# Kernel tuning notes

Hardware: AMD Instinct MI355X
Metric: run time of the kernel (lower is better)

## Reference

```python
import jax, jax.numpy as jnp
import numpy as np

# Module constants (match init_kwargs)
G = 8        # number of channel groups (len(list_input_dim))
D = 16       # per-group input dim
L = 1024     # sequence length
B = 16       # batch
E = 8        # num_experts
OUT = 64     # out_channels
KS = 3       # emb_kernel_size
K = 4        # hardcoded self.k in Channel_Embedding
LOSS_COEF = 0.01


def setup_inputs() -> dict:
    key = jax.random.key(0)
    k0, k1, k2, k3 = jax.random.split(key, 4)
    x = jax.random.normal(k0, (B, G * D, L), jnp.float32)
    # torch inits w_gate to zeros (degenerate); use small random weights for meaningful routing
    w_gate = jax.random.normal(k1, (G, D * 5, E), jnp.float32) * 0.1
    conv1_w = jax.random.normal(k2, (G, OUT, D, KS), jnp.float32) * (1.0 / np.sqrt(D * KS))
    conv1_b = jnp.zeros((G, OUT), jnp.float32)
    conv2_w = jax.random.normal(k3, (G, OUT * E, OUT, 1), jnp.float32) * (1.0 / np.sqrt(OUT))
    conv2_b = jnp.zeros((G, OUT * E), jnp.float32)
    return dict(x=x, w_gate=w_gate, conv1_w=conv1_w, conv1_b=conv1_b,
                conv2_w=conv2_w, conv2_b=conv2_b)


def _cv_squared(v):
    # torch: x.float().var() (unbiased) / (mean^2 + eps)
    v = v.astype(jnp.float32)
    return jnp.var(v, ddof=1) / (jnp.mean(v) ** 2 + 1e-10)


def _conv1d(x, w, b):
    # x [B,C,L], w [O,I,K] -> [B,O,L'] (VALID, stride 1)
    y = jax.lax.conv_general_dilated(x, w, (1,), 'VALID',
                                     dimension_numbers=('NCH', 'OIH', 'NCH'))
    return y + b[None, :, None]


def _group_forward(xg, wg, c1w, c1b, c2w, c2b):
    # xg: [B, D, L] single channel group
    Bb = xg.shape[0]
    # gating input: last timesteps [-6:-1] -> [B, D*5]
    gate_in = xg[:, :, -6:-1].reshape(Bb, -1)
    logits = jax.nn.softmax(gate_in @ wg, axis=1)           # [B, E]
    top_v, top_i = jax.lax.top_k(logits, min(K + 1, E))     # [B, K+1]
    tkv, tki = top_v[:, :K], top_i[:, :K]
    gk = tkv / (tkv.sum(1, keepdims=True) + 1e-6)
    gates = jnp.zeros_like(logits).at[jnp.arange(Bb)[:, None], tki].set(gk)  # [B, E]
    load = (gates > 0).sum(0)                               # eval path: _gates_to_load
    loss = _cv_squared(gates.sum(0)) + _cv_squared(load)
    # experts: conv(D->OUT, k=KS) -> tanh -> conv(OUT -> OUT*E, k=1)
    h = jnp.tanh(_conv1d(xg, c1w, c1b))
    raw = _conv1d(h, c2w, c2b)                              # [B, OUT*E, L']
    Lp = raw.shape[-1]
    # channel index = d*E + e (matches torch permute+reshape(B,-1,OUT,E))
    moe = jnp.einsum('bdel,be->bdl', raw.reshape(Bb, OUT, E, Lp), gates)  # [B, OUT, L']
    return moe, loss, gates


def reference(x, w_gate, conv1_w, conv1_b, conv2_w, conv2_b):
    # split channels into G groups of D: [G, B, D, L]
    xg = x.reshape(x.shape[0], G, D, x.shape[-1]).transpose(1, 0, 2, 3)
    moe, loss, gates = jax.vmap(_group_forward)(xg, w_gate, conv1_w, conv1_b, conv2_w, conv2_b)
    combine_features = moe.transpose(1, 0, 2, 3)   # [B, G, OUT, L']
    out_loss = LOSS_COEF * loss.sum()
    gates_out = gates.transpose(1, 2, 0)           # [B, E, G]
    return combine_features, out_loss, gates_out
```

## Files before the change

### kernel.cpp

```cpp
#include <hip/hip_runtime.h>
#include <hip/hip_bf16.h>

#define NG   8
#define ND   16
#define NL   1024
#define NB   16
#define NE   8
#define NOUT 64
#define NKS  3
#define NK   4
#define NLP  1022

#define OUT_LOSS  (NB*NG*NOUT*NLP)
#define OUT_GATES (OUT_LOSS + 1)

typedef short bf16x8 __attribute__((ext_vector_type(8)));
typedef float f32x4  __attribute__((ext_vector_type(4)));

__device__ __forceinline__ float tanh_fast(float x) {
    float e = exp2f(x * 2.885390081777927f);
    return 1.0f - 2.0f / (e + 1.0f);
}

__device__ __forceinline__ unsigned fbits(float a) { return __builtin_bit_cast(unsigned, a); }
__device__ __forceinline__ float resid(float a) {
    return a - __builtin_bit_cast(float, fbits(a) & 0xFFFF0000u);
}
__device__ __forceinline__ int pack2(float a, float b) {
    return (int)((fbits(a) >> 16) | (fbits(b) & 0xFFFF0000u));
}

__device__ __forceinline__ void compute_gates_f(
    const float* __restrict__ x, const float* __restrict__ wg,
    int g, int b, float gates[8])
{
    float gi[80];
    const float* xrow = x + (size_t)(b * 128 + g * 16) * 1024 + (1024 - 6);
    #pragma unroll
    for (int d = 0; d < 16; ++d) {
        #pragma unroll
        for (int tt = 0; tt < 5; ++tt) gi[d * 5 + tt] = xrow[d * 1024 + tt];
    }
    float lg[8];
    #pragma unroll
    for (int e = 0; e < 8; ++e) lg[e] = 0.f;
    const float* wgg = wg + g * 640;
    #pragma unroll
    for (int j = 0; j < 80; ++j) {
        const float v = gi[j];
        #pragma unroll
        for (int e = 0; e < 8; ++e) lg[e] = fmaf(v, wgg[j * 8 + e], lg[e]);
    }
    float mx = lg[0];
    #pragma unroll
    for (int e = 1; e < 8; ++e) mx = fmaxf(mx, lg[e]);
    float s = 0.f;
    #pragma unroll
    for (int e = 0; e < 8; ++e) { lg[e] = expf(lg[e] - mx); s += lg[e]; }
    const float invsm = 1.f / s;
    #pragma unroll
    for (int e = 0; e < 8; ++e) lg[e] *= invsm;

    int used = 0;
    float tv[4]; int ti[4];
    #pragma unroll
    for (int k = 0; k < 4; ++k) {
        float bv = -1.f; int be = 0;
        #pragma unroll
        for (int e = 0; e < 8; ++e) {
            if (!((used >> e) & 1) && lg[e] > bv) { bv = lg[e]; be = e; }
        }
        tv[k] = bv; ti[k] = be; used |= (1 << be);
    }
    const float s4 = tv[0] + tv[1] + tv[2] + tv[3];
    const float invs = 1.f / (s4 + 1e-6f);
    #pragma unroll
    for (int e = 0; e < 8; ++e) {
        float v = 0.f;
        #pragma unroll
        for (int k = 0; k < 4; ++k) if (ti[k] == e) v = tv[k] * invs;
        gates[e] = v;
    }
}

__global__ __launch_bounds__(256) void prep_kernel(
    const float* __restrict__ x,   const float* __restrict__ wg,
    const float* __restrict__ c1w, const float* __restrict__ c2w,
    const float* __restrict__ c2b,
    float* __restrict__ out, int4* __restrict__ weffA,
    float* __restrict__ beff, float* __restrict__ w1r)
{
    const int bid = blockIdx.x;
    const int t   = threadIdx.x;

    __shared__ float glds[128][8];
    __shared__ float impa[64], loda[64];
    __shared__ float lossg[8];

    if (bid < 128) {
        const int gb = bid, g = gb >> 4, b = gb & 15;
        float gt[8];
        compute_gates_f(x, wg, g, b, gt);

        const int o  = t >> 2;
        const int iq = (t & 3) * 16;
        const float* w2g = c2w + (size_t)g * 512 * 64 + (size_t)o * 8 * 64 + iq;
        float acc[16];
        #pragma unroll
        for (int q = 0; q < 16; ++q) acc[q] = 0.f;
        #pragma unroll
        for (int e = 0; e < 8; ++e) {
            const float4* src = (const float4*)(w2g + e * 64);
            #pragma unroll
            for (int q = 0; q < 4; ++q) {
                float4 v = src[q];
                acc[q*4+0] = fmaf(gt[e], v.x, acc[q*4+0]);
                acc[q*4+1] = fmaf(gt[e], v.y, acc[q*4+1]);
                acc[q*4+2] = fmaf(gt[e], v.z, acc[q*4+2]);
                acc[q*4+3] = fmaf(gt[e], v.w, acc[q*4+3]);
            }
        }
        const int mt  = o >> 4;
        const int ks  = iq >> 5;
        const int lgA = (iq & 31) >> 3;
        int4* wdst = weffA + gb * 1024 + mt * 128 + ks * 64;
        #pragma unroll
        for (int R = 0; R < 2; ++R) {
            int4 whi, wlo;
            whi.x = pack2(acc[R*8+0], acc[R*8+1]);
            whi.y = pack2(acc[R*8+2], acc[R*8+3]);
            whi.z = pack2(acc[R*8+4], acc[R*8+5]);
            whi.w = pack2(acc[R*8+6], acc[R*8+7]);
            wlo.x = pack2(resid(acc[R*8+0]), resid(acc[R*8+1]));
            wlo.y = pack2(resid(acc[R*8+2]), resid(acc[R*8+3]));
            wlo.z = pack2(resid(acc[R*8+4]), resid(acc[R*8+5]));
            wlo.w = pack2(resid(acc[R*8+6]), resid(acc[R*8+7]));
            const int slot = (lgA + R) * 16 + (o & 15);
            wdst[slot]       = whi;
            wdst[512 + slot] = wlo;
        }
        if (t < 64) {
            const float* b2g = c2b + g * 512;
            float a = 0.f;
            #pragma unroll
            for (int e = 0; e < 8; ++e) a = fmaf(gt[e], b2g[t * 8 + e], a);
            beff[gb * 64 + t] = a;
        }
    } else if (bid < 136) {
        const int g = bid - 128;
        for (int idx = t; idx < 48 * 64; idx += 256) {
            const int j = idx >> 6, o = idx & 63;
            w1r[(size_t)(g * 48 + j) * 64 + o] = c1w[(size_t)g * 3072 + o * 48 + j];
        }
    } else {
        float gates[8];
        const int g = t >> 4, b = t & 15;
        if (t < 128) {
            compute_gates_f(x, wg, g, b, gates);
            #pragma unroll
            for (int e = 0; e < 8; ++e) {
                glds[t][e] = gates[e];
                out[OUT_GATES + (b * 8 + e) * 8 + g] = gates[e];
            }
        }
        __syncthreads();
        if (t < 64) {
            const int gg = t >> 3, e = t & 7;
            float si = 0.f, sl = 0.f;
            for (int bb = 0; bb < 16; ++bb) {
                const float v = glds[gg * 16 + bb][e];
                si += v;
                sl += (v > 0.f) ? 1.f : 0.f;
            }
            impa[t] = si; loda[t] = sl;
        }
        __syncthreads();
        if (t < 8) {
            float m1 = 0.f, m2 = 0.f;
            #pragma unroll
            for (int e = 0; e < 8; ++e) { m1 += impa[t * 8 + e]; m2 += loda[t * 8 + e]; }
            m1 *= 0.125f; m2 *= 0.125f;
            float v1 = 0.f, v2 = 0.f;
            #pragma unroll
            for (int e = 0; e < 8; ++e) {
                const float d1 = impa[t * 8 + e] - m1, d2 = loda[t * 8 + e] - m2;
                v1 += d1 * d1; v2 += d2 * d2;
            }
            v1 *= (1.f / 7.f); v2 *= (1.f / 7.f);
            lossg[t] = v1 / (m1 * m1 + 1e-10f) + v2 / (m2 * m2 + 1e-10f);
        }
        __syncthreads();
        if (t == 0) {
            float tot = 0.f;
            #pragma unroll
            for (int gg = 0; gg < 8; ++gg) tot += lossg[gg];
            out[OUT_LOSS] = 0.01f * tot;
        }
    }
}

__global__ __launch_bounds__(256, 4) void main_kernel(
    const float* __restrict__ x,    const float* __restrict__ w1r,
    const float* __restrict__ b1,   const int4* __restrict__ weffA,
    const float* __restrict__ beff, float* __restrict__ out)
{
    __shared__ int4 hfrag[2048];

    const int bid   = blockIdx.x;
    const int xcd   = bid & 7;
    const int jj    = bid >> 3;
    const int gb    = ((jj & 15) << 3) | xcd;
    const int tile  = jj >> 4;
    const int g     = gb >> 4, b = gb & 15;
    const int t     = threadIdx.x;
    const int lane  = t & 63;
    const int wv    = t >> 6;
    const int obase = __builtin_amdgcn_readfirstlane(wv << 4);
    const int c0    = lane * 2;
    const int l0    = tile * 128 + c0;
    const int lc    = (l0 <= NLP - 2) ? l0 : (NLP - 2);

    float a0[16], a1[16];
    const float* b1g = b1 + g * 64 + obase;
    #pragma unroll
    for (int o = 0; o < 16; ++o) { a0[o] = b1g[o]; a1[o] = a0[o]; }

    const float* xb  = x + (size_t)(b * 128 + g * 16) * 1024 + lc;
    const float* wrg = w1r + (size_t)(g * 48) * 64 + obase;

    float2 xaA[8], xcA[8];
    #pragma unroll
    for (int i = 0; i < 8; ++i) {
        xaA[i] = *(const float2*)(xb + i * 1024);
        xcA[i] = *(const float2*)(xb + i * 1024 + 2);
    }
    float2 xaB[8], xcB[8];
    #pragma unroll
    for (int i = 0; i < 8; ++i) {
        xaB[i] = *(const float2*)(xb + (8 + i) * 1024);
        xcB[i] = *(const float2*)(xb + (8 + i) * 1024 + 2);
    }
    #pragma unroll
    for (int i = 0; i < 8; ++i) {
        const float* wr = wrg + i * 192;
        #pragma unroll
        for (int o = 0; o < 16; ++o) {
            const float w0 = wr[o], w1 = wr[64 + o], w2 = wr[128 + o];
            a0[o] = fmaf(w0, xaA[i].x, a0[o]);
            a0[o] = fmaf(w1, xaA[i].y, a0[o]);
            a0[o] = fmaf(w2, xcA[i].x, a0[o]);
            a1[o] = fmaf(w0, xaA[i].y, a1[o]);
            a1[o] = fmaf(w1, xcA[i].x, a1[o]);
            a1[o] = fmaf(w2, xcA[i].y, a1[o]);
        }
    }
    #pragma unroll
    for (int i = 0; i < 8; ++i) {
        const float* wr = wrg + (8 + i) * 192;
        #pragma unroll
        for (int o = 0; o < 16; ++o) {
            const float w0 = wr[o], w1 = wr[64 + o], w2 = wr[128 + o];
            a0[o] = fmaf(w0, xaB[i].x, a0[o]);
            a0[o] = fmaf(w1, xaB[i].y, a0[o]);
            a0[o] = fmaf(w2, xcB[i].x, a0[o]);
            a1[o] = fmaf(w0, xaB[i].y, a1[o]);
            a1[o] = fmaf(w1, xcB[i].x, a1[o]);
            a1[o] = fmaf(w2, xcB[i].y, a1[o]);
        }
    }
    #pragma unroll
    for (int o = 0; o < 16; ++o) { a0[o] = tanh_fast(a0[o]); a1[o] = tanh_fast(a1[o]); }

    {
        const int ks1 = obase >> 5;
        const int lg0 = (obase >> 3) & 3;
        #pragma unroll
        for (int cp = 0; cp < 2; ++cp) {
            const int c = c0 + cp;
            const int ub = (c >> 4) * 64 + lg0 * 16 + (c & 15);
            #pragma unroll
            for (int R = 0; R < 2; ++R) {
                float h0, h1, h2, h3, h4, h5, h6, h7;
                if (cp == 0) {
                    h0=a0[R*8+0]; h1=a0[R*8+1]; h2=a0[R*8+2]; h3=a0[R*8+3];
                    h4=a0[R*8+4]; h5=a0[R*8+5]; h6=a0[R*8+6]; h7=a0[R*8+7];
                } else {
                    h0=a1[R*8+0]; h1=a1[R*8+1]; h2=a1[R*8+2]; h3=a1[R*8+3];
                    h4=a1[R*8+4]; h5=a1[R*8+5]; h6=a1[R*8+6]; h7=a1[R*8+7];
                }
                int4 whi, wlo;
                whi.x = pack2(h0, h1); whi.y = pack2(h2, h3);
                whi.z = pack2(h4, h5); whi.w = pack2(h6, h7);
                wlo.x = pack2(resid(h0), resid(h1)); wlo.y = pack2(resid(h2), resid(h3));
                wlo.z = pack2(resid(h4), resid(h5)); wlo.w = pack2(resid(h6), resid(h7));
                hfrag[ks1 * 512 + ub + R * 16]       = whi;
                hfrag[(2 + ks1) * 512 + ub + R * 16] = wlo;
            }
        }
    }

    const int rbase = (lane >> 4) << 2;
    const float* befp = beff + gb * 64 + rbase;
    f32x4 bias0 = *(const f32x4*)(befp);
    f32x4 bias1 = *(const f32x4*)(befp + 16);
    f32x4 bias2 = *(const f32x4*)(befp + 32);
    f32x4 bias3 = *(const f32x4*)(befp + 48);

    __syncthreads();

    const int nt0 = wv * 2;
    f32x4 acc[4][2];
    acc[0][0] = bias0; acc[0][1] = bias0;
    acc[1][0] = bias1; acc[1][1] = bias1;
    acc[2][0] = bias2; acc[2][1] = bias2;
    acc[3][0] = bias3; acc[3][1] = bias3;

    const int4* wAbase = weffA + gb * 1024 + lane;
    #pragma unroll
    for (int ks = 0; ks < 2; ++ks) {
        bf16x8 Bh0 = *(const bf16x8*)&hfrag[ks * 512 + nt0 * 64 + lane];
        bf16x8 Bh1 = *(const bf16x8*)&hfrag[ks * 512 + (nt0 + 1) * 64 + lane];
        bf16x8 Bl0 = *(const bf16x8*)&hfrag[(2 + ks) * 512 + nt0 * 64 + lane];
        bf16x8 Bl1 = *(const bf16x8*)&hfrag[(2 + ks) * 512 + (nt0 + 1) * 64 + lane];
        #pragma unroll
        for (int mt = 0; mt < 4; ++mt) {
            bf16x8 Ah = *(const bf16x8*)(wAbase + mt * 128 + ks * 64);
            bf16x8 Al = *(const bf16x8*)(wAbase + 512 + mt * 128 + ks * 64);
            acc[mt][0] = __builtin_amdgcn_mfma_f32_16x16x32_bf16(Ah, Bh0, acc[mt][0], 0, 0, 0);
            acc[mt][1] = __builtin_amdgcn_mfma_f32_16x16x32_bf16(Ah, Bh1, acc[mt][1], 0, 0, 0);
            acc[mt][0] = __builtin_amdgcn_mfma_f32_16x16x32_bf16(Ah, Bl0, acc[mt][0], 0, 0, 0);
            acc[mt][1] = __builtin_amdgcn_mfma_f32_16x16x32_bf16(Ah, Bl1, acc[mt][1], 0, 0, 0);
            acc[mt][0] = __builtin_amdgcn_mfma_f32_16x16x32_bf16(Al, Bh0, acc[mt][0], 0, 0, 0);
            acc[mt][1] = __builtin_amdgcn_mfma_f32_16x16x32_bf16(Al, Bh1, acc[mt][1], 0, 0, 0);
        }
    }

    const int colg = tile * 128 + nt0 * 16 + (lane & 15);
    float* outg = out + (size_t)((b * 8 + g) * 64) * NLP;
    #pragma unroll
    for (int mt = 0; mt < 4; ++mt) {
        #pragma unroll
        for (int j = 0; j < 2; ++j) {
            const int cg = colg + j * 16;
            if (cg < NLP) {
                float* orow = outg + (size_t)(mt * 16 + rbase) * NLP + cg;
                orow[0]             = acc[mt][j][0];
                orow[(size_t)NLP]   = acc[mt][j][1];
                orow[(size_t)NLP*2] = acc[mt][j][2];
                orow[(size_t)NLP*3] = acc[mt][j][3];
            }
        }
    }
}

extern "C" void kernel_launch(void* const* d_in, const int* in_sizes, int n_in,
                              void* d_out, int out_size, void* d_ws, size_t ws_size,
                              hipStream_t stream) {
    const float* x   = (const float*)d_in[0];
    const float* wg  = (const float*)d_in[1];
    const float* c1w = (const float*)d_in[2];
    const float* c1b = (const float*)d_in[3];
    const float* c2w = (const float*)d_in[4];
    const float* c2b = (const float*)d_in[5];
    float* out = (float*)d_out;

    char* ws    = (char*)d_ws;
    int4* weffA = (int4*)ws;
    float* beff = (float*)(ws + (size_t)131072*16);
    float* w1r  = beff + 8192;

    prep_kernel<<<137, 256, 0, stream>>>(x, wg, c1w, c2w, c2b, out, weffA, beff, w1r);
    main_kernel<<<1024, 256, 0, stream>>>(x, w1r, c1b, weffA, beff, out);
}
```

Baseline: 116.5 us.

## Compute first conv on MFMA with split-bf16 weights and LDS-staged input tile

Moves the first convolution (D->OUT, kernel 3) from scalar FP32 FMAs onto bf16 MFMA, using a hi/lo bf16 split of both weights and inputs to keep near-FP32 accuracy. The prep kernel now packs the conv1 weights into MFMA A-fragment layout. The main kernel stages a transposed x tile in LDS and builds B fragments from it. The tanh output is written in per-wave fragment layout, so each wave reuses its own conv1 results for the second GEMM. This removes the heavy VALU FMA loop and the redundant per-lane global weight loads, at the cost of extra packing work, an extra LDS pass and barrier, and three MFMAs per product for the split precision.

```diff
diff --git a/kernel.cpp b/kernel.cpp
--- a/kernel.cpp
+++ b/kernel.cpp
@@ -17,6 +17,8 @@
 typedef short bf16x8 __attribute__((ext_vector_type(8)));
 typedef float f32x4  __attribute__((ext_vector_type(4)));
 
+#define MFMA16(A, B, C) __builtin_amdgcn_mfma_f32_16x16x32_bf16((A), (B), (C), 0, 0, 0)
+
 __device__ __forceinline__ float tanh_fast(float x) {
     float e = exp2f(x * 2.885390081777927f);
     return 1.0f - 2.0f / (e + 1.0f);
@@ -88,7 +90,7 @@
     const float* __restrict__ c1w, const float* __restrict__ c2w,
     const float* __restrict__ c2b,
     float* __restrict__ out, int4* __restrict__ weffA,
-    float* __restrict__ beff, float* __restrict__ w1r)
+    float* __restrict__ beff, int4* __restrict__ w1fA)
 {
     const int bid = blockIdx.x;
     const int t   = threadIdx.x;
@@ -148,9 +150,28 @@
         }
     } else if (bid < 136) {
         const int g = bid - 128;
-        for (int idx = t; idx < 48 * 64; idx += 256) {
-            const int j = idx >> 6, o = idx & 63;
-            w1r[(size_t)(g * 48 + j) * 64 + o] = c1w[(size_t)g * 3072 + o * 48 + j];
+        for (int u = t; u < 1024; u += 256) {
+            const int s    = u >> 9;
+            const int mt   = (u >> 7) & 3;
+            const int ks   = (u >> 6) & 1;
+            const int lgrp = (u >> 4) & 3;
+            const int m    = u & 15;
+            const int o    = mt * 16 + m;
+            float v[8];
+            #pragma unroll
+            for (int e = 0; e < 8; ++e) {
+                const int k = ks * 32 + lgrp * 8 + e;
+                if (k < 48) {
+                    const int tap = (k < 32) ? (k >> 4) : 2;
+                    const int i   = k & 15;
+                    const float w = c1w[((size_t)(g * 64 + o) * 16 + i) * 3 + tap];
+                    v[e] = (s == 0) ? w : resid(w);
+                } else v[e] = 0.f;
+            }
+            int4 pk;
+            pk.x = pack2(v[0], v[1]); pk.y = pack2(v[2], v[3]);
+            pk.z = pack2(v[4], v[5]); pk.w = pack2(v[6], v[7]);
+            w1fA[(size_t)g * 1024 + u] = pk;
         }
     } else {
         float gates[8];
@@ -200,154 +221,162 @@
 }
 
 __global__ __launch_bounds__(256, 4) void main_kernel(
-    const float* __restrict__ x,    const float* __restrict__ w1r,
+    const float* __restrict__ x,    const int4* __restrict__ w1fA,
     const float* __restrict__ b1,   const int4* __restrict__ weffA,
     const float* __restrict__ beff, float* __restrict__ out)
 {
     __shared__ int4 hfrag[2048];
-
-    const int bid   = blockIdx.x;
-    const int xcd   = bid & 7;
-    const int jj    = bid >> 3;
-    const int gb    = ((jj & 15) << 3) | xcd;
-    const int tile  = jj >> 4;
-    const int g     = gb >> 4, b = gb & 15;
-    const int t     = threadIdx.x;
-    const int lane  = t & 63;
-    const int wv    = t >> 6;
-    const int obase = __builtin_amdgcn_readfirstlane(wv << 4);
-    const int c0    = lane * 2;
-    const int l0    = tile * 128 + c0;
-    const int lc    = (l0 <= NLP - 2) ? l0 : (NLP - 2);
-
-    float a0[16], a1[16];
-    const float* b1g = b1 + g * 64 + obase;
-    #pragma unroll
-    for (int o = 0; o < 16; ++o) { a0[o] = b1g[o]; a1[o] = a0[o]; }
-
-    const float* xb  = x + (size_t)(b * 128 + g * 16) * 1024 + lc;
-    const float* wrg = w1r + (size_t)(g * 48) * 64 + obase;
-
-    float2 xaA[8], xcA[8];
-    #pragma unroll
-    for (int i = 0; i < 8; ++i) {
-        xaA[i] = *(const float2*)(xb + i * 1024);
-        xcA[i] = *(const float2*)(xb + i * 1024 + 2);
-    }
-    float2 xaB[8], xcB[8];
-    #pragma unroll
-    for (int i = 0; i < 8; ++i) {
-        xaB[i] = *(const float2*)(xb + (8 + i) * 1024);
-        xcB[i] = *(const float2*)(xb + (8 + i) * 1024 + 2);
-    }
-    #pragma unroll
-    for (int i = 0; i < 8; ++i) {
-        const float* wr = wrg + i * 192;
-        #pragma unroll
-        for (int o = 0; o < 16; ++o) {
-            const float w0 = wr[o], w1 = wr[64 + o], w2 = wr[128 + o];
-            a0[o] = fmaf(w0, xaA[i].x, a0[o]);
-            a0[o] = fmaf(w1, xaA[i].y, a0[o]);
-            a0[o] = fmaf(w2, xcA[i].x, a0[o]);
-            a1[o] = fmaf(w0, xaA[i].y, a1[o]);
-            a1[o] = fmaf(w1, xcA[i].x, a1[o]);
-            a1[o] = fmaf(w2, xcA[i].y, a1[o]);
-        }
-    }
-    #pragma unroll
-    for (int i = 0; i < 8; ++i) {
-        const float* wr = wrg + (8 + i) * 192;
-        #pragma unroll
-        for (int o = 0; o < 16; ++o) {
-            const float w0 = wr[o], w1 = wr[64 + o], w2 = wr[128 + o];
-            a0[o] = fmaf(w0, xaB[i].x, a0[o]);
-            a0[o] = fmaf(w1, xaB[i].y, a0[o]);
-            a0[o] = fmaf(w2, xcB[i].x, a0[o]);
-            a1[o] = fmaf(w0, xaB[i].y, a1[o]);
-            a1[o] = fmaf(w1, xcB[i].x, a1[o]);
-            a1[o] = fmaf(w2, xcB[i].y, a1[o]);
-        }
-    }
-    #pragma unroll
-    for (int o = 0; o < 16; ++o) { a0[o] = tanh_fast(a0[o]); a1[o] = tanh_fast(a1[o]); }
+    float* xtileT = (float*)hfrag;
+
+    const int bid  = blockIdx.x;
+    const int xcd  = bid & 7;
+    const int jj   = bid >> 3;
+    const int gb   = ((jj & 15) << 3) | xcd;
+    const int tile = jj >> 4;
+    const int g    = gb >> 4, b = gb & 15;
+    const int t    = threadIdx.x;
+    const int lane = t & 63;
+    const int wv   = t >> 6;
+    const int col  = lane & 15;
+    const int j4   = lane >> 4;
+    const int l0   = tile * 128;
 
     {
-        const int ks1 = obase >> 5;
-        const int lg0 = (obase >> 3) & 3;
-        #pragma unroll
-        for (int cp = 0; cp < 2; ++cp) {
-            const int c = c0 + cp;
-            const int ub = (c >> 4) * 64 + lg0 * 16 + (c & 15);
-            #pragma unroll
-            for (int R = 0; R < 2; ++R) {
-                float h0, h1, h2, h3, h4, h5, h6, h7;
-                if (cp == 0) {
-                    h0=a0[R*8+0]; h1=a0[R*8+1]; h2=a0[R*8+2]; h3=a0[R*8+3];
-                    h4=a0[R*8+4]; h5=a0[R*8+5]; h6=a0[R*8+6]; h7=a0[R*8+7];
-                } else {
-                    h0=a1[R*8+0]; h1=a1[R*8+1]; h2=a1[R*8+2]; h3=a1[R*8+3];
-                    h4=a1[R*8+4]; h5=a1[R*8+5]; h6=a1[R*8+6]; h7=a1[R*8+7];
-                }
-                int4 whi, wlo;
-                whi.x = pack2(h0, h1); whi.y = pack2(h2, h3);
-                whi.z = pack2(h4, h5); whi.w = pack2(h6, h7);
-                wlo.x = pack2(resid(h0), resid(h1)); wlo.y = pack2(resid(h2), resid(h3));
-                wlo.z = pack2(resid(h4), resid(h5)); wlo.w = pack2(resid(h6), resid(h7));
-                hfrag[ks1 * 512 + ub + R * 16]       = whi;
-                hfrag[(2 + ks1) * 512 + ub + R * 16] = wlo;
-            }
-        }
-    }
-
-    const int rbase = (lane >> 4) << 2;
+        const int si  = t >> 4;
+        const int sc0 = t & 15;
+        const float* xr = x + (size_t)(b * 128 + g * 16 + si) * 1024;
+        #pragma unroll
+        for (int kk = 0; kk < 9; ++kk) {
+            const int c = sc0 + kk * 16;
+            if (c < 130) {
+                int gc = l0 + c; if (gc > 1023) gc = 1023;
+                xtileT[c * 20 + si] = xr[gc];
+            }
+        }
+    }
+    __syncthreads();
+
+    bf16x8 B1h[2][2], B1l[2][2];
+    #pragma unroll
+    for (int tl = 0; tl < 2; ++tl) {
+        #pragma unroll
+        for (int ks = 0; ks < 2; ++ks) {
+            const int tap = (ks == 0) ? (j4 >> 1) : 2;
+            const int i0  = (j4 & 1) * 8;
+            const bool valid = (ks == 0) || (j4 < 2);
+            const int c = (wv * 2 + tl) * 16 + col;
+            const float* p = &xtileT[(c + tap) * 20 + i0];
+            float v[8];
+            *(float4*)&v[0] = *(const float4*)p;
+            *(float4*)&v[4] = *(const float4*)(p + 4);
+            #pragma unroll
+            for (int e = 0; e < 8; ++e) if (!valid) v[e] = 0.f;
+            int4 bh, bl;
+            bh.x = pack2(v[0], v[1]); bh.y = pack2(v[2], v[3]);
+            bh.z = pack2(v[4], v[5]); bh.w = pack2(v[6], v[7]);
+            bl.x = pack2(resid(v[0]), resid(v[1])); bl.y = pack2(resid(v[2]), resid(v[3]));
+            bl.z = pack2(resid(v[4]), resid(v[5])); bl.w = pack2(resid(v[6]), resid(v[7]));
+            B1h[tl][ks] = __builtin_bit_cast(bf16x8, bh);
+            B1l[tl][ks] = __builtin_bit_cast(bf16x8, bl);
+        }
+    }
+    __syncthreads();
+
+    const int rbase = j4 << 2;
+    f32x4 acc1[2][4];
+    #pragma unroll
+    for (int mt = 0; mt < 4; ++mt) {
+        f32x4 bv = *(const f32x4*)(b1 + g * 64 + mt * 16 + rbase);
+        acc1[0][mt] = bv; acc1[1][mt] = bv;
+    }
+    const int4* w1base = w1fA + g * 1024 + lane;
+    #pragma unroll
+    for (int mt = 0; mt < 4; ++mt) {
+        bf16x8 Ah0 = *(const bf16x8*)(w1base + mt * 128);
+        bf16x8 Ah1 = *(const bf16x8*)(w1base + mt * 128 + 64);
+        bf16x8 Al0 = *(const bf16x8*)(w1base + 512 + mt * 128);
+        bf16x8 Al1 = *(const bf16x8*)(w1base + 512 + mt * 128 + 64);
+        #pragma unroll
+        for (int tl = 0; tl < 2; ++tl) {
+            f32x4 a = acc1[tl][mt];
+            a = MFMA16(Ah0, B1h[tl][0], a);
+            a = MFMA16(Ah0, B1l[tl][0], a);
+            a = MFMA16(Al0, B1h[tl][0], a);
+            a = MFMA16(Ah1, B1h[tl][1], a);
+            a = MFMA16(Ah1, B1l[tl][1], a);
+            a = MFMA16(Al1, B1h[tl][1], a);
+            acc1[tl][mt] = a;
+        }
+    }
+
+    {
+        char* base = (char*)hfrag;
+        const int wb  = wv * 512;
+        const int lgt0 = j4 >> 1;
+        const int woff = (j4 & 1) * 8;
+        #pragma unroll
+        for (int tl = 0; tl < 2; ++tl) {
+            #pragma unroll
+            for (int mt = 0; mt < 4; ++mt) {
+                const float t0 = tanh_fast(acc1[tl][mt][0]);
+                const float t1 = tanh_fast(acc1[tl][mt][1]);
+                const float t2 = tanh_fast(acc1[tl][mt][2]);
+                const float t3 = tanh_fast(acc1[tl][mt][3]);
+                const int kst = mt >> 1;
+                const int lgt = ((mt & 1) << 1) + lgt0;
+                const int uhi = wb + kst * 128 + tl * 64 + lgt * 16 + col;
+                uint2 whi, wlo;
+                whi.x = (unsigned)pack2(t0, t1);
+                whi.y = (unsigned)pack2(t2, t3);
+                wlo.x = (unsigned)pack2(resid(t0), resid(t1));
+                wlo.y = (unsigned)pack2(resid(t2), resid(t3));
+                *(uint2*)(base + uhi * 16 + woff)         = whi;
+                *(uint2*)(base + (uhi + 256) * 16 + woff) = wlo;
+            }
+        }
+    }
+
+    f32x4 acc2[4][2];
     const float* befp = beff + gb * 64 + rbase;
-    f32x4 bias0 = *(const f32x4*)(befp);
-    f32x4 bias1 = *(const f32x4*)(befp + 16);
-    f32x4 bias2 = *(const f32x4*)(befp + 32);
-    f32x4 bias3 = *(const f32x4*)(befp + 48);
-
-    __syncthreads();
-
-    const int nt0 = wv * 2;
-    f32x4 acc[4][2];
-    acc[0][0] = bias0; acc[0][1] = bias0;
-    acc[1][0] = bias1; acc[1][1] = bias1;
-    acc[2][0] = bias2; acc[2][1] = bias2;
-    acc[3][0] = bias3; acc[3][1] = bias3;
-
+    #pragma unroll
+    for (int mt = 0; mt < 4; ++mt) {
+        f32x4 bv = *(const f32x4*)(befp + mt * 16);
+        acc2[mt][0] = bv; acc2[mt][1] = bv;
+    }
     const int4* wAbase = weffA + gb * 1024 + lane;
     #pragma unroll
     for (int ks = 0; ks < 2; ++ks) {
-        bf16x8 Bh0 = *(const bf16x8*)&hfrag[ks * 512 + nt0 * 64 + lane];
-        bf16x8 Bh1 = *(const bf16x8*)&hfrag[ks * 512 + (nt0 + 1) * 64 + lane];
-        bf16x8 Bl0 = *(const bf16x8*)&hfrag[(2 + ks) * 512 + nt0 * 64 + lane];
-        bf16x8 Bl1 = *(const bf16x8*)&hfrag[(2 + ks) * 512 + (nt0 + 1) * 64 + lane];
+        const int wb = wv * 512;
+        bf16x8 Bh0 = *(const bf16x8*)&hfrag[wb + ks * 128 + lane];
+        bf16x8 Bh1 = *(const bf16x8*)&hfrag[wb + ks * 128 + 64 + lane];
+        bf16x8 Bl0 = *(const bf16x8*)&hfrag[wb + (2 + ks) * 128 + lane];
+        bf16x8 Bl1 = *(const bf16x8*)&hfrag[wb + (2 + ks) * 128 + 64 + lane];
         #pragma unroll
         for (int mt = 0; mt < 4; ++mt) {
             bf16x8 Ah = *(const bf16x8*)(wAbase + mt * 128 + ks * 64);
             bf16x8 Al = *(const bf16x8*)(wAbase + 512 + mt * 128 + ks * 64);
-            acc[mt][0] = __builtin_amdgcn_mfma_f32_16x16x32_bf16(Ah, Bh0, acc[mt][0], 0, 0, 0);
-            acc[mt][1] = __builtin_amdgcn_mfma_f32_16x16x32_bf16(Ah, Bh1, acc[mt][1], 0, 0, 0);
-            acc[mt][0] = __builtin_amdgcn_mfma_f32_16x16x32_bf16(Ah, Bl0, acc[mt][0], 0, 0, 0);
-            acc[mt][1] = __builtin_amdgcn_mfma_f32_16x16x32_bf16(Ah, Bl1, acc[mt][1], 0, 0, 0);
-            acc[mt][0] = __builtin_amdgcn_mfma_f32_16x16x32_bf16(Al, Bh0, acc[mt][0], 0, 0, 0);
-            acc[mt][1] = __builtin_amdgcn_mfma_f32_16x16x32_bf16(Al, Bh1, acc[mt][1], 0, 0, 0);
-        }
-    }
-
-    const int colg = tile * 128 + nt0 * 16 + (lane & 15);
+            acc2[mt][0] = MFMA16(Ah, Bh0, acc2[mt][0]);
+            acc2[mt][1] = MFMA16(Ah, Bh1, acc2[mt][1]);
+            acc2[mt][0] = MFMA16(Ah, Bl0, acc2[mt][0]);
+            acc2[mt][1] = MFMA16(Ah, Bl1, acc2[mt][1]);
+            acc2[mt][0] = MFMA16(Al, Bh0, acc2[mt][0]);
+            acc2[mt][1] = MFMA16(Al, Bh1, acc2[mt][1]);
+        }
+    }
+
+    const int colg = l0 + wv * 32 + col;
     float* outg = out + (size_t)((b * 8 + g) * 64) * NLP;
     #pragma unroll
     for (int mt = 0; mt < 4; ++mt) {
         #pragma unroll
-        for (int j = 0; j < 2; ++j) {
-            const int cg = colg + j * 16;
+        for (int tl = 0; tl < 2; ++tl) {
+            const int cg = colg + tl * 16;
             if (cg < NLP) {
                 float* orow = outg + (size_t)(mt * 16 + rbase) * NLP + cg;
-                orow[0]             = acc[mt][j][0];
-                orow[(size_t)NLP]   = acc[mt][j][1];
-                orow[(size_t)NLP*2] = acc[mt][j][2];
-                orow[(size_t)NLP*3] = acc[mt][j][3];
+                orow[0]             = acc2[mt][tl][0];
+                orow[(size_t)NLP]   = acc2[mt][tl][1];
+                orow[(size_t)NLP*2] = acc2[mt][tl][2];
+                orow[(size_t)NLP*3] = acc2[mt][tl][3];
             }
         }
     }
@@ -366,9 +395,9 @@
 
     char* ws    = (char*)d_ws;
     int4* weffA = (int4*)ws;
-    float* beff = (float*)(ws + (size_t)131072*16);
-    float* w1r  = beff + 8192;
-
-    prep_kernel<<<137, 256, 0, stream>>>(x, wg, c1w, c2w, c2b, out, weffA, beff, w1r);
-    main_kernel<<<1024, 256, 0, stream>>>(x, w1r, c1b, weffA, beff, out);
-}
+    int4* w1fA  = weffA + 131072;
+    float* beff = (float*)(w1fA + 8192);
+
+    prep_kernel<<<137, 256, 0, stream>>>(x, wg, c1w, c2w, c2b, out, weffA, beff, w1fA);
+    main_kernel<<<1024, 256, 0, stream>>>(x, w1fA, c1b, weffA, beff, out);
+}
```

New measurement: 110.6 us. 1.05x faster.
